# Optimization experiments

Hardware: AMD Instinct MI355X
Metric: run time of the kernel (lower is better)

The kernel has to match this reference:

```python
import jax, jax.numpy as jnp
import numpy as np

B, C, H, W = 16, 128, 128, 128
NUM_HEADS, HEAD_DIM = 4, 32
HIDDEN = NUM_HEADS * HEAD_DIM  # 128
GROUPS = 32
EPS = 1e-5


def setup_inputs() -> dict:
    key = jax.random.key(0)
    ks = jax.random.split(key, 6)
    # conv1x1 weights: torch Conv2d weight (out, in, 1, 1) -> stored as (out, in)
    fan_qkv = C
    fan_proj = HIDDEN
    return {
        "x": jax.random.normal(ks[0], (B, C, H, W), dtype=jnp.float32),
        "gn_w": jnp.ones((C,), dtype=jnp.float32),
        "gn_b": jnp.zeros((C,), dtype=jnp.float32),
        "qkv_w": jax.random.normal(ks[1], (3 * HIDDEN, C), dtype=jnp.float32) / np.sqrt(fan_qkv),
        "proj_w": jax.random.normal(ks[2], (C, HIDDEN), dtype=jnp.float32) / np.sqrt(fan_proj),
        "proj_b": jax.random.normal(ks[3], (C,), dtype=jnp.float32) * 0.01,
    }


def reference(x, gn_w, gn_b, qkv_w, proj_w, proj_b):
    b, c, h, w = x.shape
    n = h * w
    residual = x
    # GroupNorm(32 groups), biased variance, affine
    xg = x.reshape(b, GROUPS, c // GROUPS, h, w)
    mu = xg.mean(axis=(2, 3, 4), keepdims=True)
    var = xg.var(axis=(2, 3, 4), keepdims=True)
    xn = ((xg - mu) * jax.lax.rsqrt(var + EPS)).reshape(b, c, h, w)
    xn = xn * gn_w[None, :, None, None] + gn_b[None, :, None, None]
    # 1x1 conv QKV (no bias); channel layout -> (b, 3, heads, head_dim, n)
    qkv = jnp.einsum('oc,bchw->bohw', qkv_w, xn)
    qkv = qkv.reshape(b, 3, NUM_HEADS, HEAD_DIM, n)
    q, k, v = qkv[:, 0], qkv[:, 1], qkv[:, 2]
    q = jax.nn.softmax(q, axis=-1)   # over spatial positions
    k = jax.nn.softmax(k, axis=-2)   # over head_dim
    # context = k @ v^T : (b,h,D,D)
    ctx = jnp.einsum('bhdn,bhen->bhde', k, v)
    # out = context^T @ q : (b,h,D,n)
    out = jnp.einsum('bhde,bhdn->bhen', ctx, q)
    out = out.reshape(b, HIDDEN, h, w)
    # 1x1 conv projection (with bias)
    out = jnp.einsum('co,bohw->bchw', proj_w, out) + proj_b[None, :, None, None]
    return out + residual
```

## Files before the change

kernel.cpp:

```cpp
#include <hip/hip_runtime.h>


#define B_ 16
#define C_ 128
#define N_ 16384

typedef short bf16x8 __attribute__((ext_vector_type(8)));
typedef float f32x4 __attribute__((ext_vector_type(4)));
typedef unsigned u32x2 __attribute__((ext_vector_type(2)));

__device__ __forceinline__ ushort f2bf(float f) {
    union { float f; unsigned u; } v; v.f = f;
    unsigned r = (v.u + 0x7FFFu + ((v.u >> 16) & 1u)) >> 16;
    return (ushort)r;
}
__device__ __forceinline__ float bf2f(unsigned h) {
    union { unsigned u; float f; } v; v.u = h << 16;
    return v.f;
}

__global__ void k_stats(const float* __restrict__ x, const float* __restrict__ gnw,
                        const float* __restrict__ gnb, float* __restrict__ sc,
                        float* __restrict__ bi,
                        const float* __restrict__ qkvw, ushort* __restrict__ wbf) {
    int bg = blockIdx.x;
    if (bg >= 512) {
        int i = (bg - 512) * 1024 + threadIdx.x;
        if (i < 384 * 128) wbf[i] = f2bf(qkvw[i]);
        return;
    }
    const float4* p = (const float4*)(x + (size_t)bg * (4 * N_));
    float s = 0.f, s2 = 0.f;
    for (int i = threadIdx.x; i < N_; i += 1024) {
        float4 v = p[i];
        s  += v.x + v.y + v.z + v.w;
        s2 += v.x * v.x + v.y * v.y + v.z * v.z + v.w * v.w;
    }
    #pragma unroll
    for (int d = 32; d > 0; d >>= 1) { s += __shfl_xor(s, d); s2 += __shfl_xor(s2, d); }
    __shared__ float ls[16], ls2[16];
    int wid = threadIdx.x >> 6, lane = threadIdx.x & 63;
    if (lane == 0) { ls[wid] = s; ls2[wid] = s2; }
    __syncthreads();
    if (threadIdx.x == 0) {
        float S = 0.f, S2 = 0.f;
        #pragma unroll
        for (int i = 0; i < 16; ++i) { S += ls[i]; S2 += ls2[i]; }
        float m = S / 65536.f;
        float var = S2 / 65536.f - m * m;
        float rs = rsqrtf(var + 1e-5f);
        int b = bg >> 5, g = bg & 31;
        #pragma unroll
        for (int i = 0; i < 4; ++i) {
            int c = g * 4 + i;
            float scv = rs * gnw[c];
            sc[b * 128 + c] = scv;
            bi[b * 128 + c] = gnb[c] - m * scv;
        }
    }
}


#define MFMA16(A, Bv, Cc) __builtin_amdgcn_mfma_f32_16x16x32_bf16(A, Bv, Cc, 0, 0, 0)

#define DO_Q(J) do { \
    f32x4 acc = {0.f, 0.f, 0.f, 0.f}; \
    acc = MFMA16(wf[J][0], xb[0], acc); acc = MFMA16(wf[J][1], xb[1], acc); \
    acc = MFMA16(wf[J][2], xb[2], acc); acc = MFMA16(wf[J][3], xb[3], acc); \
    qacc[J][0] += __expf(acc[0]); qacc[J][1] += __expf(acc[1]); \
    qacc[J][2] += __expf(acc[2]); qacc[J][3] += __expf(acc[3]); \
} while (0)

#define DO_K(JLO, H) do { \
    f32x4 aL = {0.f, 0.f, 0.f, 0.f}, aH = {0.f, 0.f, 0.f, 0.f}; \
    aL = MFMA16(wf[JLO][0], xb[0], aL);     aH = MFMA16(wf[(JLO)+1][0], xb[0], aH); \
    aL = MFMA16(wf[JLO][1], xb[1], aL);     aH = MFMA16(wf[(JLO)+1][1], xb[1], aH); \
    aL = MFMA16(wf[JLO][2], xb[2], aL);     aH = MFMA16(wf[(JLO)+1][2], xb[2], aH); \
    aL = MFMA16(wf[JLO][3], xb[3], aL);     aH = MFMA16(wf[(JLO)+1][3], xb[3], aH); \
    float eL0 = __expf(aL[0]), eL1 = __expf(aL[1]), eL2 = __expf(aL[2]), eL3 = __expf(aL[3]); \
    float eH0 = __expf(aH[0]), eH1 = __expf(aH[1]), eH2 = __expf(aH[2]), eH3 = __expf(aH[3]); \
    float s = eL0 + eL1 + eL2 + eL3 + eH0 + eH1 + eH2 + eH3; \
    s += __shfl_xor(s, 16); s += __shfl_xor(s, 32); \
    float rinv = 1.f / s; \
    ksm[H][lg * 4 + 0][nloc] = f2bf(eL0 * rinv); \
    ksm[H][lg * 4 + 1][nloc] = f2bf(eL1 * rinv); \
    ksm[H][lg * 4 + 2][nloc] = f2bf(eL2 * rinv); \
    ksm[H][lg * 4 + 3][nloc] = f2bf(eL3 * rinv); \
    ksm[H][16 + lg * 4 + 0][nloc] = f2bf(eH0 * rinv); \
    ksm[H][16 + lg * 4 + 1][nloc] = f2bf(eH1 * rinv); \
    ksm[H][16 + lg * 4 + 2][nloc] = f2bf(eH2 * rinv); \
    ksm[H][16 + lg * 4 + 3][nloc] = f2bf(eH3 * rinv); \
} while (0)

#define DO_V(J, HV, EB) do { \
    f32x4 acc = {0.f, 0.f, 0.f, 0.f}; \
    acc = MFMA16(wf[J][0], xb[0], acc); acc = MFMA16(wf[J][1], xb[1], acc); \
    acc = MFMA16(wf[J][2], xb[2], acc); acc = MFMA16(wf[J][3], xb[3], acc); \
    vls[HV][(EB) + lg * 4 + 0][nloc] = f2bf(acc[0]); \
    vls[HV][(EB) + lg * 4 + 1][nloc] = f2bf(acc[1]); \
    vls[HV][(EB) + lg * 4 + 2][nloc] = f2bf(acc[2]); \
    vls[HV][(EB) + lg * 4 + 3][nloc] = f2bf(acc[3]); \
} while (0)

#define DO_CTX() do { \
    bf16x8 A0 = *(const bf16x8*)&ksm[wid][l15][lg * 8]; \
    bf16x8 A1 = *(const bf16x8*)&ksm[wid][16 + l15][lg * 8]; \
    bf16x8 B0 = *(const bf16x8*)&vls[wid][l15][lg * 8]; \
    bf16x8 B1 = *(const bf16x8*)&vls[wid][16 + l15][lg * 8]; \
    cacc[0][0] = MFMA16(A0, B0, cacc[0][0]); \
    cacc[0][1] = MFMA16(A0, B1, cacc[0][1]); \
    cacc[1][0] = MFMA16(A1, B0, cacc[1][0]); \
    cacc[1][1] = MFMA16(A1, B1, cacc[1][1]); \
} while (0)

__global__ __launch_bounds__(256, 2) void k_main(
    const float* __restrict__ x, const ushort* __restrict__ wbf,
    const float* __restrict__ scA, const float* __restrict__ biA,
    float* __restrict__ qsumP, float* __restrict__ ctxP) {
    int blk = blockIdx.x;
    int b = blk >> 6, nb = blk & 63;
    int tid = threadIdx.x, wid = tid >> 6, lane = tid & 63;
    int l15 = lane & 15, lg = lane >> 4;

    __shared__ __align__(16) ushort xs[4096];
    __shared__ __align__(16) ushort ksm[4][32][40];
    __shared__ __align__(16) ushort vls[4][32][40];

    bf16x8 wf[6][4];
    {
        const ushort* wr = wbf + (size_t)(wid * 96 + l15) * 128 + lg * 8;
        #pragma unroll
        for (int j = 0; j < 6; ++j)
            #pragma unroll
            for (int kc = 0; kc < 4; ++kc)
                wf[j][kc] = *(const bf16x8*)(wr + j * 2048 + kc * 32);
    }

    float qacc[6][4];
    #pragma unroll
    for (int j = 0; j < 6; ++j)
        #pragma unroll
        for (int r = 0; r < 4; ++r) qacc[j][r] = 0.f;
    f32x4 cacc[2][2];
    #pragma unroll
    for (int di = 0; di < 2; ++di)
        #pragma unroll
        for (int ei = 0; ei < 2; ++ei) cacc[di][ei] = (f32x4){0.f, 0.f, 0.f, 0.f};

    const int pk_ = tid & 7, pcb = tid >> 3;
    const float* xrow = x + (size_t)b * (C_ * N_) + nb * 256 + pk_ * 4;
    float scv[4], biv[4];
    #pragma unroll
    for (int i = 0; i < 4; ++i) {
        scv[i] = scA[b * 128 + pcb * 4 + i];
        biv[i] = biA[b * 128 + pcb * 4 + i];
    }
    unsigned boffj[4];
    #pragma unroll
    for (int j = 0; j < 4; ++j) {
        int n = pk_ * 4 + j;
        boffj[j] = (unsigned)(n * 256 + (((pcb >> 1) * 16) ^ ((n & 7) << 4)) + (pcb & 1) * 8);
    }

    float4 vbuf[4];
    #pragma unroll
    for (int i = 0; i < 4; ++i)
        vbuf[i] = *(const float4*)(xrow + (size_t)(pcb * 4 + i) * N_);

    for (int ch = 0; ch < 8; ++ch) {
        __syncthreads();
        unsigned e[4][4];
        #pragma unroll
        for (int i = 0; i < 4; ++i) {
            float s = scv[i], t = biv[i];
            e[i][0] = f2bf(vbuf[i].x * s + t);
            e[i][1] = f2bf(vbuf[i].y * s + t);
            e[i][2] = f2bf(vbuf[i].z * s + t);
            e[i][3] = f2bf(vbuf[i].w * s + t);
        }
        if (ch < 7) {
            #pragma unroll
            for (int i = 0; i < 4; ++i)
                vbuf[i] = *(const float4*)(xrow + (size_t)(pcb * 4 + i) * N_ + (ch + 1) * 32);
        }
        #pragma unroll
        for (int j = 0; j < 4; ++j) {
            u32x2 wj;
            wj.x = e[0][j] | (e[1][j] << 16);
            wj.y = e[2][j] | (e[3][j] << 16);
            *(u32x2*)((char*)xs + boffj[j]) = wj;
        }
        if (ch > 0) DO_CTX();
        __syncthreads();

        #pragma unroll
        for (int nt = 0; nt < 2; ++nt) {
            int row = nt * 16 + l15;
            bf16x8 xb[4];
            #pragma unroll
            for (int kc = 0; kc < 4; ++kc) {
                unsigned off = (unsigned)(row * 256 +
                    (((kc * 4 + lg) * 16) ^ ((row & 7) << 4)));
                xb[kc] = *(const bf16x8*)((const char*)xs + off);
            }
            int nloc = nt * 16 + l15;

            if (wid == 0) {
                DO_Q(0); DO_Q(1); DO_Q(2); DO_Q(3); DO_Q(4); DO_Q(5);
            } else if (wid == 1) {
                DO_Q(0); DO_Q(1); DO_K(2, 0); DO_K(4, 1);
            } else if (wid == 2) {
                DO_K(0, 2); DO_K(2, 3); DO_V(4, 0, 0); DO_V(5, 0, 16);
            } else {
                DO_V(0, 1, 0); DO_V(1, 1, 16); DO_V(2, 2, 0);
                DO_V(3, 2, 16); DO_V(4, 3, 0); DO_V(5, 3, 16);
            }
        }
    }
    __syncthreads();
    DO_CTX();

    int nq = (wid == 0) ? 6 : (wid == 1 ? 2 : 0);
    #pragma unroll
    for (int j = 0; j < 6; ++j) {
        if (j < nq) {
            #pragma unroll
            for (int r = 0; r < 4; ++r) {
                float s = qacc[j][r];
                s += __shfl_xor(s, 1); s += __shfl_xor(s, 2);
                s += __shfl_xor(s, 4); s += __shfl_xor(s, 8);
                if (l15 == 0)
                    qsumP[(size_t)blk * 128 + (wid * 6 + j) * 16 + lg * 4 + r] = s;
            }
        }
    }
    float* cp = ctxP + (size_t)blk * 4096 + wid * 1024;
    #pragma unroll
    for (int di = 0; di < 2; ++di)
        #pragma unroll
        for (int ei = 0; ei < 2; ++ei)
            #pragma unroll
            for (int r = 0; r < 4; ++r)
                cp[(di * 16 + lg * 4 + r) * 32 + ei * 16 + l15] = cacc[di][ei][r];
}

__global__ __launch_bounds__(1024) void k_comb(
    const float* __restrict__ ctxP, const float* __restrict__ qsumP,
    const float* __restrict__ projw, ushort* __restrict__ mpp) {
    int b = blockIdx.x, tid = threadIdx.x;
    __shared__ float ctx[4096];
    __shared__ float qinv[128];
    const float* base = ctxP + (size_t)b * 64 * 4096;
    #pragma unroll
    for (int r = 0; r < 4; ++r) {
        int i = r * 1024 + tid;
        float s = 0.f;
        for (int q = 0; q < 64; ++q) s += base[(size_t)q * 4096 + i];
        ctx[i] = s;
    }
    if (tid < 128) {
        float s = 0.f;
        const float* p = qsumP + (size_t)b * 64 * 128 + tid;
        for (int q = 0; q < 64; ++q) s += p[q * 128];
        qinv[tid] = 1.f / s;
    }
    __syncthreads();
    if (tid < 256) {
        int c = tid >> 1, hd0 = (tid & 1) * 64;
        unsigned ow[32];
        for (int k = 0; k < 64; ++k) {
            int hd = hd0 + k, h = hd >> 5, d = hd & 31;
            const float* pw = projw + c * 128 + h * 32;
            const float* cx = ctx + h * 1024 + d * 32;
            float s = 0.f;
            #pragma unroll 8
            for (int e = 0; e < 32; ++e) s += pw[e] * cx[e];
            s *= qinv[hd];
            ushort bv = f2bf(s);
            if (k & 1) ow[k >> 1] |= ((unsigned)bv) << 16; else ow[k >> 1] = bv;
        }
        ushort* dst = mpp + ((size_t)(b * 128 + c)) * 128 + hd0;
        #pragma unroll
        for (int q = 0; q < 8; ++q) {
            uint4 t; t.x = ow[q * 4]; t.y = ow[q * 4 + 1];
            t.z = ow[q * 4 + 2]; t.w = ow[q * 4 + 3];
            ((uint4*)dst)[q] = t;
        }
    }
}

__global__ __launch_bounds__(256) void k_final(
    const ushort* __restrict__ wbf, const ushort* __restrict__ mpp,
    const float* __restrict__ scA, const float* __restrict__ biA,
    const float* __restrict__ projb, const float* __restrict__ x,
    float* __restrict__ out) {
    int blk = blockIdx.x;
    int b = blk >> 8, nb = blk & 255;
    int tid = threadIdx.x, wid = tid >> 6, lane = tid & 63;
    int l15 = lane & 15, lg = lane >> 4;
    int n0 = nb * 64;

    __shared__ __align__(16) char lds[32768];
    ushort* xs   = (ushort*)lds;
    ushort* att  = (ushort*)lds;
    ushort* eqls = (ushort*)(lds + 16384);

    bf16x8 wq[2][4];
    #pragma unroll
    for (int j = 0; j < 2; ++j) {
        const ushort* wr = wbf + (size_t)((wid * 2 + j) * 16 + l15) * 128 + lg * 8;
        #pragma unroll
        for (int kc = 0; kc < 4; ++kc) wq[j][kc] = *(const bf16x8*)(wr + kc * 32);
    }
    bf16x8 bm[2][4];
    #pragma unroll
    for (int ctk = 0; ctk < 2; ++ctk) {
        const ushort* br = mpp + ((size_t)(b * 128 + (wid * 2 + ctk) * 16 + l15)) * 128 + lg * 8;
        #pragma unroll
        for (int kc = 0; kc < 4; ++kc) bm[ctk][kc] = *(const bf16x8*)(br + kc * 32);
    }

    const int pk_ = tid & 15, pcb = tid >> 4;
    float4 xv[8];
    {
        const float* xrow = x + (size_t)b * (C_ * N_) + n0 + pk_ * 4;
        unsigned e[8][4];
        #pragma unroll
        for (int i = 0; i < 8; ++i) {
            int c = pcb * 8 + i;
            float s = scA[b * 128 + c], t = biA[b * 128 + c];
            xv[i] = *(const float4*)(xrow + (size_t)c * N_);
            e[i][0] = f2bf(xv[i].x * s + t);
            e[i][1] = f2bf(xv[i].y * s + t);
            e[i][2] = f2bf(xv[i].z * s + t);
            e[i][3] = f2bf(xv[i].w * s + t);
        }
        #pragma unroll
        for (int j = 0; j < 4; ++j) {
            int n = pk_ * 4 + j;
            uint4 wj;
            wj.x = e[0][j] | (e[1][j] << 16);
            wj.y = e[2][j] | (e[3][j] << 16);
            wj.z = e[4][j] | (e[5][j] << 16);
            wj.w = e[6][j] | (e[7][j] << 16);
            unsigned byte = (unsigned)(n * 256 + ((pcb * 16) ^ ((n & 7) << 4)));
            *(uint4*)((char*)xs + byte) = wj;
        }
    }
    __syncthreads();

    #pragma unroll
    for (int nt = 0; nt < 4; ++nt) {
        int row = nt * 16 + l15;
        bf16x8 xb[4];
        #pragma unroll
        for (int kc = 0; kc < 4; ++kc) {
            unsigned off = (unsigned)(row * 256 + (((kc * 4 + lg) * 16) ^ ((row & 7) << 4)));
            xb[kc] = *(const bf16x8*)((const char*)xs + off);
        }
        #pragma unroll
        for (int j = 0; j < 2; ++j) {
            f32x4 a = {0.f, 0.f, 0.f, 0.f};
            #pragma unroll
            for (int kc = 0; kc < 4; ++kc) a = MFMA16(wq[j][kc], xb[kc], a);
            u32x2 pk;
            pk.x = (unsigned)f2bf(__expf(a[0])) | ((unsigned)f2bf(__expf(a[1])) << 16);
            pk.y = (unsigned)f2bf(__expf(a[2])) | ((unsigned)f2bf(__expf(a[3])) << 16);
            int ot = wid * 2 + j;
            unsigned byte = (unsigned)(row * 256 +
                (((ot * 2 + (lg >> 1)) * 16) ^ ((row & 7) << 4)) + (lg & 1) * 8);
            *(u32x2*)((char*)eqls + byte) = pk;
        }
    }
    __syncthreads();

    #pragma unroll
    for (int nt = 0; nt < 4; ++nt) {
        int row = nt * 16 + l15;
        bf16x8 af[4];
        #pragma unroll
        for (int kc = 0; kc < 4; ++kc) {
            unsigned off = (unsigned)(row * 256 + (((kc * 4 + lg) * 16) ^ ((row & 7) << 4)));
            af[kc] = *(const bf16x8*)((const char*)eqls + off);
        }
        #pragma unroll
        for (int ctk = 0; ctk < 2; ++ctk) {
            f32x4 a = {0.f, 0.f, 0.f, 0.f};
            #pragma unroll
            for (int kc = 0; kc < 4; ++kc) a = MFMA16(af[kc], bm[ctk][kc], a);
            int c = (wid * 2 + ctk) * 16 + l15;
            u32x2 pk;
            pk.x = (unsigned)f2bf(a[0]) | ((unsigned)f2bf(a[1]) << 16);
            pk.y = (unsigned)f2bf(a[2]) | ((unsigned)f2bf(a[3]) << 16);
            unsigned byte = (unsigned)(c * 128 +
                (((nt * 2 + (lg >> 1)) * 16) ^ ((c & 7) << 4)) + (lg & 1) * 8);
            *(u32x2*)((char*)att + byte) = pk;
        }
    }
    __syncthreads();

    {
        size_t obase = (size_t)b * (C_ * N_) + n0 + pk_ * 4;
        #pragma unroll
        for (int i = 0; i < 8; ++i) {
            int c = pcb * 8 + i;
            unsigned byte = (unsigned)(c * 128 +
                (((pk_ >> 1) * 16) ^ ((c & 7) << 4)) + (pk_ & 1) * 8);
            u32x2 pk = *(const u32x2*)((const char*)att + byte);
            float pbv = projb[c];
            f32x4 o4;
            o4[0] = bf2f(pk.x & 0xffffu) + pbv + xv[i].x;
            o4[1] = bf2f(pk.x >> 16)     + pbv + xv[i].y;
            o4[2] = bf2f(pk.y & 0xffffu) + pbv + xv[i].z;
            o4[3] = bf2f(pk.y >> 16)     + pbv + xv[i].w;
            *(f32x4*)(out + obase + (size_t)c * N_) = o4;
        }
    }
}

extern "C" void kernel_launch(void* const* d_in, const int* in_sizes, int n_in,
                              void* d_out, int out_size, void* d_ws, size_t ws_size,
                              hipStream_t stream) {
    const float* x     = (const float*)d_in[0];
    const float* gnw   = (const float*)d_in[1];
    const float* gnb   = (const float*)d_in[2];
    const float* qkvw  = (const float*)d_in[3];
    const float* projw = (const float*)d_in[4];
    const float* projb = (const float*)d_in[5];
    float* out = (float*)d_out;

    char* ws = (char*)d_ws;
    ushort* wbf   = (ushort*)(ws);
    float*  qsumP = (float*)(ws + 102400);
    ushort* mpp   = (ushort*)(ws + 626688);
    float*  sc    = (float*)(ws + 1150976);
    float*  bi    = (float*)(ws + 1159168);
    float*  ctxP  = (float*)(ws + 1167360);

    k_stats<<<560,  1024, 0, stream>>>(x, gnw, gnb, sc, bi, qkvw, wbf);
    k_main <<<1024, 256,  0, stream>>>(x, wbf, sc, bi, qsumP, ctxP);
    k_comb <<<16,   1024, 0, stream>>>(ctxP, qsumP, projw, mpp);
    k_final<<<4096, 256,  0, stream>>>(wbf, mpp, sc, bi, projb, x, out);
}
```

Before: 216.1 us.

## Make k_final persistent over four tiles with double-buffered LDS and prefetch

k_final now processes four 64-position tiles per block (1024 blocks instead of 4096), so weight and ctx fragment loads are amortized across tiles. Each iteration prefetches the next tile's x into registers and writes the previous tile's output while the current tile is staged, using ping-pong LDS buffers. The residual x is re-read from global memory at output time instead of being kept in registers, which adds extra global reads. Fewer blocks may reduce latency hiding across the GPU.

```diff
diff --git a/kernel.cpp b/kernel.cpp
--- a/kernel.cpp
+++ b/kernel.cpp
@@ -17,6 +17,9 @@
 __device__ __forceinline__ float bf2f(unsigned h) {
     union { unsigned u; float f; } v; v.u = h << 16;
     return v.f;
+}
+__device__ __forceinline__ float fc4(const float4& v, int j) {
+    return j == 0 ? v.x : (j == 1 ? v.y : (j == 2 ? v.z : v.w));
 }
 
 __global__ void k_stats(const float* __restrict__ x, const float* __restrict__ gnw,
@@ -59,7 +62,6 @@
         }
     }
 }
-
 
 #define MFMA16(A, Bv, Cc) __builtin_amdgcn_mfma_f32_16x16x32_bf16(A, Bv, Cc, 0, 0, 0)
 
@@ -295,15 +297,11 @@
     const float* __restrict__ projb, const float* __restrict__ x,
     float* __restrict__ out) {
     int blk = blockIdx.x;
-    int b = blk >> 8, nb = blk & 255;
+    int b = blk >> 6, nb = blk & 63;
     int tid = threadIdx.x, wid = tid >> 6, lane = tid & 63;
     int l15 = lane & 15, lg = lane >> 4;
-    int n0 = nb * 64;
 
     __shared__ __align__(16) char lds[32768];
-    ushort* xs   = (ushort*)lds;
-    ushort* att  = (ushort*)lds;
-    ushort* eqls = (ushort*)(lds + 16384);
 
     bf16x8 wq[2][4];
     #pragma unroll
@@ -321,98 +319,144 @@
     }
 
     const int pk_ = tid & 15, pcb = tid >> 4;
+    const float* xrow = x + (size_t)b * (C_ * N_) + nb * 256 + pk_ * 4;
+    float scv[8], biv[8];
+    #pragma unroll
+    for (int i = 0; i < 8; ++i) {
+        int c = pcb * 8 + i;
+        scv[i] = scA[b * 128 + c];
+        biv[i] = biA[b * 128 + c];
+    }
+
     float4 xv[8];
-    {
-        const float* xrow = x + (size_t)b * (C_ * N_) + n0 + pk_ * 4;
-        unsigned e[8][4];
-        #pragma unroll
-        for (int i = 0; i < 8; ++i) {
-            int c = pcb * 8 + i;
-            float s = scA[b * 128 + c], t = biA[b * 128 + c];
-            xv[i] = *(const float4*)(xrow + (size_t)c * N_);
-            e[i][0] = f2bf(xv[i].x * s + t);
-            e[i][1] = f2bf(xv[i].y * s + t);
-            e[i][2] = f2bf(xv[i].z * s + t);
-            e[i][3] = f2bf(xv[i].w * s + t);
-        }
+    #pragma unroll
+    for (int i = 0; i < 8; ++i)
+        xv[i] = *(const float4*)(xrow + (size_t)(pcb * 8 + i) * N_);
+
+    for (int t = 0; t < 4; ++t) {
+        char* bufX = lds + (t & 1) * 16384;
+        char* bufE = lds + ((t + 1) & 1) * 16384;
+
+        f32x4 xr[8];
+        if (t > 0) {
+            const float* rrow = xrow + (t - 1) * 64;
+            #pragma unroll
+            for (int i = 0; i < 8; ++i)
+                xr[i] = *(const f32x4*)(rrow + (size_t)(pcb * 8 + i) * N_);
+        }
+
         #pragma unroll
         for (int j = 0; j < 4; ++j) {
             int n = pk_ * 4 + j;
             uint4 wj;
-            wj.x = e[0][j] | (e[1][j] << 16);
-            wj.y = e[2][j] | (e[3][j] << 16);
-            wj.z = e[4][j] | (e[5][j] << 16);
-            wj.w = e[6][j] | (e[7][j] << 16);
+            wj.x = (unsigned)f2bf(fc4(xv[0], j) * scv[0] + biv[0]) |
+                   ((unsigned)f2bf(fc4(xv[1], j) * scv[1] + biv[1]) << 16);
+            wj.y = (unsigned)f2bf(fc4(xv[2], j) * scv[2] + biv[2]) |
+                   ((unsigned)f2bf(fc4(xv[3], j) * scv[3] + biv[3]) << 16);
+            wj.z = (unsigned)f2bf(fc4(xv[4], j) * scv[4] + biv[4]) |
+                   ((unsigned)f2bf(fc4(xv[5], j) * scv[5] + biv[5]) << 16);
+            wj.w = (unsigned)f2bf(fc4(xv[6], j) * scv[6] + biv[6]) |
+                   ((unsigned)f2bf(fc4(xv[7], j) * scv[7] + biv[7]) << 16);
             unsigned byte = (unsigned)(n * 256 + ((pcb * 16) ^ ((n & 7) << 4)));
-            *(uint4*)((char*)xs + byte) = wj;
-        }
-    }
-    __syncthreads();
-
-    #pragma unroll
-    for (int nt = 0; nt < 4; ++nt) {
-        int row = nt * 16 + l15;
-        bf16x8 xb[4];
-        #pragma unroll
-        for (int kc = 0; kc < 4; ++kc) {
-            unsigned off = (unsigned)(row * 256 + (((kc * 4 + lg) * 16) ^ ((row & 7) << 4)));
-            xb[kc] = *(const bf16x8*)((const char*)xs + off);
-        }
-        #pragma unroll
-        for (int j = 0; j < 2; ++j) {
-            f32x4 a = {0.f, 0.f, 0.f, 0.f};
-            #pragma unroll
-            for (int kc = 0; kc < 4; ++kc) a = MFMA16(wq[j][kc], xb[kc], a);
-            u32x2 pk;
-            pk.x = (unsigned)f2bf(__expf(a[0])) | ((unsigned)f2bf(__expf(a[1])) << 16);
-            pk.y = (unsigned)f2bf(__expf(a[2])) | ((unsigned)f2bf(__expf(a[3])) << 16);
-            int ot = wid * 2 + j;
-            unsigned byte = (unsigned)(row * 256 +
-                (((ot * 2 + (lg >> 1)) * 16) ^ ((row & 7) << 4)) + (lg & 1) * 8);
-            *(u32x2*)((char*)eqls + byte) = pk;
-        }
-    }
-    __syncthreads();
-
-    #pragma unroll
-    for (int nt = 0; nt < 4; ++nt) {
-        int row = nt * 16 + l15;
-        bf16x8 af[4];
-        #pragma unroll
-        for (int kc = 0; kc < 4; ++kc) {
-            unsigned off = (unsigned)(row * 256 + (((kc * 4 + lg) * 16) ^ ((row & 7) << 4)));
-            af[kc] = *(const bf16x8*)((const char*)eqls + off);
-        }
-        #pragma unroll
-        for (int ctk = 0; ctk < 2; ++ctk) {
-            f32x4 a = {0.f, 0.f, 0.f, 0.f};
-            #pragma unroll
-            for (int kc = 0; kc < 4; ++kc) a = MFMA16(af[kc], bm[ctk][kc], a);
-            int c = (wid * 2 + ctk) * 16 + l15;
-            u32x2 pk;
-            pk.x = (unsigned)f2bf(a[0]) | ((unsigned)f2bf(a[1]) << 16);
-            pk.y = (unsigned)f2bf(a[2]) | ((unsigned)f2bf(a[3]) << 16);
-            unsigned byte = (unsigned)(c * 128 +
-                (((nt * 2 + (lg >> 1)) * 16) ^ ((c & 7) << 4)) + (lg & 1) * 8);
-            *(u32x2*)((char*)att + byte) = pk;
-        }
-    }
-    __syncthreads();
+            *(uint4*)(bufX + byte) = wj;
+        }
+        if (t < 3) {
+            const float* prow = xrow + (t + 1) * 64;
+            #pragma unroll
+            for (int i = 0; i < 8; ++i)
+                xv[i] = *(const float4*)(prow + (size_t)(pcb * 8 + i) * N_);
+        }
+        if (t > 0) {
+            char* bufD = lds + ((t - 1) & 1) * 16384;
+            size_t obase = (size_t)b * (C_ * N_) + nb * 256 + (t - 1) * 64 + pk_ * 4;
+            #pragma unroll
+            for (int i = 0; i < 8; ++i) {
+                int c = pcb * 8 + i;
+                unsigned byte = (unsigned)(c * 128 +
+                    (((pk_ >> 1) * 16) ^ ((c & 7) << 4)) + (pk_ & 1) * 8);
+                u32x2 pk = *(const u32x2*)(bufD + byte);
+                float pbv = projb[c];
+                f32x4 o4;
+                o4[0] = bf2f(pk.x & 0xffffu) + pbv + xr[i][0];
+                o4[1] = bf2f(pk.x >> 16)     + pbv + xr[i][1];
+                o4[2] = bf2f(pk.y & 0xffffu) + pbv + xr[i][2];
+                o4[3] = bf2f(pk.y >> 16)     + pbv + xr[i][3];
+                *(f32x4*)(out + obase + (size_t)c * N_) = o4;
+            }
+        }
+        __syncthreads();
+
+        #pragma unroll
+        for (int nt = 0; nt < 4; ++nt) {
+            int row = nt * 16 + l15;
+            bf16x8 xb[4];
+            #pragma unroll
+            for (int kc = 0; kc < 4; ++kc) {
+                unsigned off = (unsigned)(row * 256 + (((kc * 4 + lg) * 16) ^ ((row & 7) << 4)));
+                xb[kc] = *(const bf16x8*)(bufX + off);
+            }
+            #pragma unroll
+            for (int j = 0; j < 2; ++j) {
+                f32x4 a = {0.f, 0.f, 0.f, 0.f};
+                #pragma unroll
+                for (int kc = 0; kc < 4; ++kc) a = MFMA16(wq[j][kc], xb[kc], a);
+                u32x2 pk;
+                pk.x = (unsigned)f2bf(__expf(a[0])) | ((unsigned)f2bf(__expf(a[1])) << 16);
+                pk.y = (unsigned)f2bf(__expf(a[2])) | ((unsigned)f2bf(__expf(a[3])) << 16);
+                int ot = wid * 2 + j;
+                unsigned byte = (unsigned)(row * 256 +
+                    (((ot * 2 + (lg >> 1)) * 16) ^ ((row & 7) << 4)) + (lg & 1) * 8);
+                *(u32x2*)(bufE + byte) = pk;
+            }
+        }
+        __syncthreads();
+
+        #pragma unroll
+        for (int nt = 0; nt < 4; ++nt) {
+            int row = nt * 16 + l15;
+            bf16x8 af[4];
+            #pragma unroll
+            for (int kc = 0; kc < 4; ++kc) {
+                unsigned off = (unsigned)(row * 256 + (((kc * 4 + lg) * 16) ^ ((row & 7) << 4)));
+                af[kc] = *(const bf16x8*)(bufE + off);
+            }
+            #pragma unroll
+            for (int ctk = 0; ctk < 2; ++ctk) {
+                f32x4 a = {0.f, 0.f, 0.f, 0.f};
+                #pragma unroll
+                for (int kc = 0; kc < 4; ++kc) a = MFMA16(af[kc], bm[ctk][kc], a);
+                int c = (wid * 2 + ctk) * 16 + l15;
+                u32x2 pk;
+                pk.x = (unsigned)f2bf(a[0]) | ((unsigned)f2bf(a[1]) << 16);
+                pk.y = (unsigned)f2bf(a[2]) | ((unsigned)f2bf(a[3]) << 16);
+                unsigned byte = (unsigned)(c * 128 +
+                    (((nt * 2 + (lg >> 1)) * 16) ^ ((c & 7) << 4)) + (lg & 1) * 8);
+                *(u32x2*)(bufX + byte) = pk;
+            }
+        }
+        __syncthreads();
+    }
 
     {
-        size_t obase = (size_t)b * (C_ * N_) + n0 + pk_ * 4;
+        char* bufD = lds + 16384;
+        const float* rrow = xrow + 3 * 64;
+        f32x4 xr[8];
+        #pragma unroll
+        for (int i = 0; i < 8; ++i)
+            xr[i] = *(const f32x4*)(rrow + (size_t)(pcb * 8 + i) * N_);
+        size_t obase = (size_t)b * (C_ * N_) + nb * 256 + 3 * 64 + pk_ * 4;
         #pragma unroll
         for (int i = 0; i < 8; ++i) {
             int c = pcb * 8 + i;
             unsigned byte = (unsigned)(c * 128 +
                 (((pk_ >> 1) * 16) ^ ((c & 7) << 4)) + (pk_ & 1) * 8);
-            u32x2 pk = *(const u32x2*)((const char*)att + byte);
+            u32x2 pk = *(const u32x2*)(bufD + byte);
             float pbv = projb[c];
             f32x4 o4;
-            o4[0] = bf2f(pk.x & 0xffffu) + pbv + xv[i].x;
-            o4[1] = bf2f(pk.x >> 16)     + pbv + xv[i].y;
-            o4[2] = bf2f(pk.y & 0xffffu) + pbv + xv[i].z;
-            o4[3] = bf2f(pk.y >> 16)     + pbv + xv[i].w;
+            o4[0] = bf2f(pk.x & 0xffffu) + pbv + xr[i][0];
+            o4[1] = bf2f(pk.x >> 16)     + pbv + xr[i][1];
+            o4[2] = bf2f(pk.y & 0xffffu) + pbv + xr[i][2];
+            o4[3] = bf2f(pk.y >> 16)     + pbv + xr[i][3];
             *(f32x4*)(out + obase + (size_t)c * N_) = o4;
         }
     }
@@ -440,5 +484,5 @@
     k_stats<<<560,  1024, 0, stream>>>(x, gnw, gnb, sc, bi, qkvw, wbf);
     k_main <<<1024, 256,  0, stream>>>(x, wbf, sc, bi, qsumP, ctxP);
     k_comb <<<16,   1024, 0, stream>>>(ctxP, qsumP, projw, mpp);
-    k_final<<<4096, 256,  0, stream>>>(wbf, mpp, sc, bi, projb, x, out);
-}
+    k_final<<<1024, 256,  0, stream>>>(wbf, mpp, sc, bi, projb, x, out);
+}
```

Result: slower. 221.8 us (+2.6%).
